# Kernel tuning notes

Measured on AMD Instinct MI355X. Metric: run time of the kernel, lower is better.

## Reference

```python
import jax, jax.numpy as jnp
import numpy as np

B = 8
H1c = W1c = 56
H2c = W2c = 112
C1 = 512
C2 = 256
NH = 8
WS = 7
POOL = 2
EPS = 1e-5


def setup_inputs() -> dict:
    key = jax.random.key(0)
    ks = jax.random.split(key, 8)
    x = jax.random.normal(ks[0], (B, H1c * W1c, C1), dtype=jnp.float32)
    y = jax.random.normal(ks[1], (B, H2c * W2c, C2), dtype=jnp.float32)
    Wq = jax.random.normal(ks[2], (C1, C1), dtype=jnp.float32) * 0.02
    Wkv = jax.random.normal(ks[3], (2 * C1, C2), dtype=jnp.float32) * 0.02
    Wproj = jax.random.normal(ks[4], (C1, C1), dtype=jnp.float32) * 0.02
    bproj = jnp.zeros((C1,), dtype=jnp.float32)
    # 1x1 conv: fan_out = out_channels -> std = sqrt(2/C2)
    Wsr = jax.random.normal(ks[5], (C2, C2), dtype=jnp.float32) * np.sqrt(2.0 / C2).astype(np.float32)
    bsr = jnp.zeros((C2,), dtype=jnp.float32)
    gn = jnp.ones((C2,), dtype=jnp.float32)
    bn = jnp.zeros((C2,), dtype=jnp.float32)
    return {"x": x, "y": y, "Wq": Wq, "Wkv": Wkv, "Wproj": Wproj,
            "bproj": bproj, "Wsr": Wsr, "bsr": bsr, "gn": gn, "bn": bn,
            "H1": H1c, "W1": W1c, "H2": H2c, "W2": W2c}


def _window_partition(t, ws):
    # t: (B, nh, H, W, C) -> (B*nh, num_windows, ws*ws, C)
    Bt, n, H, W, C = t.shape
    ht, wt = H // ws, W // ws
    t = t.reshape(Bt, n, ht, ws, wt, ws, C).transpose(0, 1, 2, 4, 3, 5, 6)
    return t.reshape(Bt * n, ht * wt, ws * ws, C)


def reference(x, y, Wq, Wkv, Wproj, bproj, Wsr, bsr, gn, bn, H1, W1, H2, W2):
    B1, N1, c1 = x.shape
    B2, N2, c2 = y.shape
    nh, ws = NH, WS
    hd = c1 // nh
    scale = hd ** (-0.5)

    # q projection -> (B, nh, H1, W1, hd)
    q = (x @ Wq.T).reshape(B1, H1, W1, nh, hd).transpose(0, 3, 1, 2, 4)

    # KV preprocessing: avgpool -> 1x1 conv -> layernorm -> gelu
    y2 = y.transpose(0, 2, 1).reshape(B2, c2, H2, W2)
    Hp, Wp = H2 // POOL, W2 // POOL
    y2 = y2.reshape(B2, c2, Hp, POOL, Wp, POOL).mean(axis=(3, 5))
    y2 = jnp.einsum('bchw,oc->bohw', y2, Wsr) + bsr[None, :, None, None]
    y2 = y2.reshape(B2, c2, Hp * Wp).transpose(0, 2, 1)  # (B, Np, C2)
    mu = y2.mean(-1, keepdims=True)
    var = y2.var(-1, keepdims=True)
    y2 = (y2 - mu) / jnp.sqrt(var + EPS) * gn + bn
    y2 = jax.nn.gelu(y2, approximate=False)

    kv = (y2 @ Wkv.T).reshape(B2, Hp * Wp, 2, nh, hd)
    k = kv[:, :, 0].transpose(0, 2, 1, 3).reshape(B2, nh, Hp, Wp, hd)
    v = kv[:, :, 1].transpose(0, 2, 1, 3).reshape(B2, nh, Hp, Wp, hd)

    qw = _window_partition(q, ws)   # (B*nh, nw, ws^2, hd)
    kw = _window_partition(k, ws)
    vw = _window_partition(v, ws)

    attn = jax.nn.softmax(jnp.einsum('bnqd,bnkd->bnqk', qw, kw) * scale, axis=-1)
    out = jnp.einsum('bnqk,bnkd->bnqd', attn, vw)  # (B*nh, nw, ws^2, hd)

    # window reverse -> (B, N1, C1)
    ht, wt = H1 // ws, W1 // ws
    out = out.reshape(B1, nh, ht, wt, ws, ws, hd).transpose(0, 1, 2, 4, 3, 5, 6)
    out = out.reshape(B1, nh, H1 * W1, hd).transpose(0, 2, 1, 3).reshape(B1, H1 * W1, c1)
    return out @ Wproj.T + bproj
```

## Files before the change

### kernel.cpp

```cpp
#include <hip/hip_runtime.h>
#include <hip/hip_bf16.h>

typedef __attribute__((ext_vector_type(8))) short short8;
typedef __attribute__((ext_vector_type(4))) float f32x4;
typedef __attribute__((ext_vector_type(4))) unsigned short ushort4v;

#define DI __device__ __forceinline__

DI unsigned short f2bf(float f) {
  union { float f; unsigned int u; } a; a.f = f;
  unsigned int u = a.u;
  return (unsigned short)((u + 0x7FFFu + ((u >> 16) & 1u)) >> 16);
}

#define BARRIER() do { asm volatile("" ::: "memory"); __builtin_amdgcn_s_barrier(); asm volatile("" ::: "memory"); } while (0)
#define GLOAD16(src, dst) __builtin_amdgcn_global_load_lds( \
    (const __attribute__((address_space(1))) void*)(src), \
    (__attribute__((address_space(3))) void*)(dst), 16, 0, 0)


__global__ __launch_bounds__(256)
void cvt_pool(const float* __restrict__ y, unsigned short* __restrict__ pooled,
              const float* __restrict__ Wq, const float* __restrict__ Wkv,
              const float* __restrict__ Wproj, const float* __restrict__ Wsr,
              unsigned short* __restrict__ Wq_b, unsigned short* __restrict__ Wkv_b,
              unsigned short* __restrict__ Wproj_b, unsigned short* __restrict__ Wsr_b) {
  int bid = blockIdx.x;
  if (bid < 6272) {
    int t = bid * 256 + threadIdx.x;
    int cv = (t & 63) * 4;
    int bp = t >> 6;
    int b = bp / 3136, p = bp % 3136;
    int hp = p / 56, wp = p % 56;
    const float* src = y + (((size_t)b * 12544) + hp * 224 + wp * 2) * 256 + cv;
    float4 a0 = *(const float4*)(src);
    float4 a1 = *(const float4*)(src + 256);
    float4 a2 = *(const float4*)(src + 28672);
    float4 a3 = *(const float4*)(src + 28672 + 256);
    float4 av;
    av.x = (a0.x + a1.x + a2.x + a3.x) * 0.25f;
    av.y = (a0.y + a1.y + a2.y + a3.y) * 0.25f;
    av.z = (a0.z + a1.z + a2.z + a3.z) * 0.25f;
    av.w = (a0.w + a1.w + a2.w + a3.w) * 0.25f;
    ushort4v o = { f2bf(av.x), f2bf(av.y), f2bf(av.z), f2bf(av.w) };
    *(ushort4v*)&pooled[(size_t)bp * 256 + cv] = o;
  } else {
    long i = (long)(bid - 6272) * 1024 + threadIdx.x * 4;
    const float* src; unsigned short* dst; long off;
    if (i < 262144L)      { src = Wq;    dst = Wq_b;    off = i; }
    else if (i < 524288L) { src = Wkv;   dst = Wkv_b;   off = i - 262144L; }
    else if (i < 786432L) { src = Wproj; dst = Wproj_b; off = i - 524288L; }
    else                  { src = Wsr;   dst = Wsr_b;   off = i - 786432L; }
    float4 v = *(const float4*)&src[off];
    ushort4v o = { f2bf(v.x), f2bf(v.y), f2bf(v.z), f2bf(v.w) };
    *(ushort4v*)&dst[off] = o;
  }
}

__global__ __launch_bounds__(256)
void sr_gemm(const unsigned short* __restrict__ Ap, const unsigned short* __restrict__ Wsr_b,
             const float* __restrict__ bsr, const float* __restrict__ gn,
             const float* __restrict__ bn, unsigned short* __restrict__ out) {
  __shared__ unsigned short sA[64 * 64];
  __shared__ unsigned short sB[256 * 64];
  __shared__ float red[64 * 8];

  const int tid = threadIdx.x;
  const int wv = tid >> 6;
  const int lane = tid & 63;
  const int lr = lane & 15;
  const int lg = lane >> 4;
  const int lr4 = lg * 4;
  const int m0 = blockIdx.x * 64;
  const int sr8 = lane >> 3;
  const int sl8 = lane & 7;

  f32x4 acc[4][4];
#pragma unroll
  for (int i = 0; i < 4; ++i)
#pragma unroll
    for (int j = 0; j < 4; ++j) acc[i][j] = (f32x4){0.f, 0.f, 0.f, 0.f};

  for (int kt = 0; kt < 256; kt += 64) {
#pragma unroll
    for (int c = 0; c < 2; ++c) {
      int row = wv * 16 + c * 8 + sr8;
      GLOAD16(Ap + (size_t)(m0 + row) * 256 + kt + ((sl8 ^ (row & 7)) * 8),
              &sA[(wv * 16 + c * 8) * 64]);
    }
#pragma unroll
    for (int c = 0; c < 8; ++c) {
      int row = wv * 64 + c * 8 + sr8;
      GLOAD16(Wsr_b + (size_t)row * 256 + kt + ((sl8 ^ (row & 7)) * 8),
              &sB[(wv * 64 + c * 8) * 64]);
    }
    __syncthreads();
#pragma unroll
    for (int ks = 0; ks < 2; ++ks) {
      short8 af[4], bfr[4];
#pragma unroll
      for (int i = 0; i < 4; ++i)
        af[i] = *(const short8*)&sA[(i * 16 + lr) * 64 + (((ks * 4 + lg) ^ (lr & 7)) * 8)];
#pragma unroll
      for (int j = 0; j < 4; ++j)
        bfr[j] = *(const short8*)&sB[(wv * 64 + j * 16 + lr) * 64 + (((ks * 4 + lg) ^ (lr & 7)) * 8)];
#pragma unroll
      for (int i = 0; i < 4; ++i)
#pragma unroll
        for (int j = 0; j < 4; ++j)
          acc[i][j] = __builtin_amdgcn_mfma_f32_16x16x32_bf16(af[i], bfr[j], acc[i][j], 0, 0, 0);
    }
    __syncthreads();
  }

  float bsv[4], gnv[4], bnv[4];
#pragma unroll
  for (int j = 0; j < 4; ++j) {
    int col = wv * 64 + j * 16 + lr;
    bsv[j] = bsr[col]; gnv[j] = gn[col]; bnv[j] = bn[col];
  }
  float s_[4][4], q_[4][4];
#pragma unroll
  for (int i = 0; i < 4; ++i)
#pragma unroll
    for (int r = 0; r < 4; ++r) {
      float s = 0.f, q = 0.f;
#pragma unroll
      for (int j = 0; j < 4; ++j) {
        float v = acc[i][j][r] + bsv[j];
        acc[i][j][r] = v;
        s += v; q += v * v;
      }
      s_[i][r] = s; q_[i][r] = q;
    }
#pragma unroll
  for (int m = 1; m <= 8; m <<= 1)
#pragma unroll
    for (int i = 0; i < 4; ++i)
#pragma unroll
      for (int r = 0; r < 4; ++r) {
        s_[i][r] += __shfl_xor(s_[i][r], m);
        q_[i][r] += __shfl_xor(q_[i][r], m);
      }
  if (lr == 0) {
#pragma unroll
    for (int i = 0; i < 4; ++i)
#pragma unroll
      for (int r = 0; r < 4; ++r) {
        int row = i * 16 + lr4 + r;
        red[row * 8 + wv * 2 + 0] = s_[i][r];
        red[row * 8 + wv * 2 + 1] = q_[i][r];
      }
  }
  __syncthreads();
#pragma unroll
  for (int i = 0; i < 4; ++i) {
#pragma unroll
    for (int r = 0; r < 4; ++r) {
      int row = i * 16 + lr4 + r;
      float sum = red[row * 8 + 0] + red[row * 8 + 2] + red[row * 8 + 4] + red[row * 8 + 6];
      float sq  = red[row * 8 + 1] + red[row * 8 + 3] + red[row * 8 + 5] + red[row * 8 + 7];
      float mean = sum * (1.f / 256.f);
      float var = sq * (1.f / 256.f) - mean * mean;
      float rstd = rsqrtf(var + 1e-5f);
#pragma unroll
      for (int j = 0; j < 4; ++j) {
        float t = (acc[i][j][r] - mean) * rstd * gnv[j] + bnv[j];
        t = 0.5f * t * (1.f + erff(t * 0.70710678118654752f));
        out[(size_t)(m0 + row) * 256 + wv * 64 + j * 16 + lr] = f2bf(t);
      }
    }
  }
}

template<int N, int EPI>
DI void epi_store(int gm, int gc, float v, void* outp, const float* bias, unsigned short* out2) {
  if constexpr (EPI == 3) {
    ((float*)outp)[(size_t)gm * N + gc] = v + bias[gc];
  } else if constexpr (EPI == 0) {
    const int b = gm / 3136, pos = gm % 3136;
    const int h = pos / 56, ww = pos % 56;
    const int head = gc >> 6, d = gc & 63;
    const size_t idx = ((((size_t)(b * 8 + head)) * 64 + (h / 7) * 8 + (ww / 7)) * 49
                        + (h % 7) * 7 + (ww % 7)) * 64 + d;
    ((unsigned short*)outp)[idx] = f2bf(v);
  }
}

template<int K, int N, int EPI>
__global__ __launch_bounds__(512, 2)
void gemm256f(const float* __restrict__ A,
              const unsigned short* __restrict__ Bw,
              void* __restrict__ outp,
              const float* __restrict__ bias,
              unsigned short* __restrict__ out2) {
  __shared__ unsigned short lds[65536];
  const int tid = threadIdx.x;
  const int wv = tid >> 6;
  const int lane = tid & 63;
  const int wm = wv >> 2;
  const int wn = wv & 3;
  const int m0 = blockIdx.y * 256;
  const int n0 = blockIdx.x * 256;
  const int lr = lane & 15;
  const int lg = lane >> 4;
  const int lr4 = lg * 4;
  const int srow8 = lane >> 3;
  const int sl8 = lane & 7;
  constexpr int NT = K / 64;

  f32x4 acc[8][4];
#pragma unroll
  for (int i = 0; i < 8; ++i)
#pragma unroll
    for (int j = 0; j < 4; ++j) acc[i][j] = (f32x4){0.f, 0.f, 0.f, 0.f};

  float4 fa[4][2];
  auto loadA = [&](int t1) {
    int tsrc = (t1 < NT) ? t1 : NT - 1;
#pragma unroll
    for (int rr = 0; rr < 4; ++rr) {
      int trow = rr * 64 + wv * 8 + srow8;
      const float* p = A + (size_t)(m0 + trow) * K + tsrc * 64 + sl8 * 8;
      fa[rr][0] = *(const float4*)p;
      fa[rr][1] = *(const float4*)(p + 4);
    }
    asm volatile("" ::: "memory");
  };
  auto writeA = [&](int t1) {
#pragma unroll
    for (int rr = 0; rr < 4; ++rr) {
      int trow = rr * 64 + wv * 8 + srow8;
      union { short8 s; unsigned short u[8]; } w;
      w.u[0] = f2bf(fa[rr][0].x); w.u[1] = f2bf(fa[rr][0].y);
      w.u[2] = f2bf(fa[rr][0].z); w.u[3] = f2bf(fa[rr][0].w);
      w.u[4] = f2bf(fa[rr][1].x); w.u[5] = f2bf(fa[rr][1].y);
      w.u[6] = f2bf(fa[rr][1].z); w.u[7] = f2bf(fa[rr][1].w);
      *(short8*)&lds[(t1 & 1) * 32768 + trow * 64 + ((sl8 ^ (trow & 7)) * 8)] = w.s;
    }
  };
  auto stageB = [&](int t1, int rr) {
    int tsrc = (t1 < NT) ? t1 : NT - 1;
    int trow = rr * 64 + wv * 8 + srow8;
    int sx = sl8 ^ (trow & 7);
    GLOAD16(Bw + (size_t)(n0 + trow) * K + tsrc * 64 + sx * 8,
            &lds[(t1 & 1) * 32768 + 16384 + (rr * 64 + wv * 8) * 64]);
  };
  auto rdA = [&](int s, int mf, int ks) -> short8 {
    int row = wm * 128 + mf * 16 + lr;
    int slot = ((ks << 2) + lg) ^ (row & 7);
    return *(const short8*)&lds[s * 32768 + row * 64 + slot * 8];
  };
  auto rdB = [&](int s, int nf, int ks) -> short8 {
    int row = wn * 64 + nf * 16 + lr;
    int slot = ((ks << 2) + lg) ^ (row & 7);
    return *(const short8*)&lds[s * 32768 + 16384 + row * 64 + slot * 8];
  };

  stageB(0, 0); stageB(0, 1); stageB(0, 2); stageB(0, 3);
  loadA(0);
  asm volatile("s_waitcnt vmcnt(0)" ::: "memory");
  writeA(0);
  asm volatile("s_waitcnt lgkmcnt(0)" ::: "memory");
  BARRIER();

  for (int t = 0; t < NT; ++t) {
    const int s = t & 1;
    short8 bfr[4][2];
    loadA(t + 1);
#pragma unroll
    for (int j = 0; j < 4; ++j) { bfr[j][0] = rdB(s, j, 0); bfr[j][1] = rdB(s, j, 1); }
    {
      short8 x0 = rdA(s, 0, 0), x1 = rdA(s, 0, 1);
      short8 y0 = rdA(s, 1, 0), y1 = rdA(s, 1, 1);
      BARRIER();
      __builtin_amdgcn_s_setprio(1);
#pragma unroll
      for (int j = 0; j < 4; ++j) {
        acc[0][j] = __builtin_amdgcn_mfma_f32_16x16x32_bf16(x0, bfr[j][0], acc[0][j], 0, 0, 0);
        acc[0][j] = __builtin_amdgcn_mfma_f32_16x16x32_bf16(x1, bfr[j][1], acc[0][j], 0, 0, 0);
        acc[1][j] = __builtin_amdgcn_mfma_f32_16x16x32_bf16(y0, bfr[j][0], acc[1][j], 0, 0, 0);
        acc[1][j] = __builtin_amdgcn_mfma_f32_16x16x32_bf16(y1, bfr[j][1], acc[1][j], 0, 0, 0);
      }
      __builtin_amdgcn_s_setprio(0);
      BARRIER();
    }
    stageB(t + 1, 0); stageB(t + 1, 1);
    {
      short8 x0 = rdA(s, 2, 0), x1 = rdA(s, 2, 1);
      short8 y0 = rdA(s, 3, 0), y1 = rdA(s, 3, 1);
      BARRIER();
      __builtin_amdgcn_s_setprio(1);
#pragma unroll
      for (int j = 0; j < 4; ++j) {
        acc[2][j] = __builtin_amdgcn_mfma_f32_16x16x32_bf16(x0, bfr[j][0], acc[2][j], 0, 0, 0);
        acc[2][j] = __builtin_amdgcn_mfma_f32_16x16x32_bf16(x1, bfr[j][1], acc[2][j], 0, 0, 0);
        acc[3][j] = __builtin_amdgcn_mfma_f32_16x16x32_bf16(y0, bfr[j][0], acc[3][j], 0, 0, 0);
        acc[3][j] = __builtin_amdgcn_mfma_f32_16x16x32_bf16(y1, bfr[j][1], acc[3][j], 0, 0, 0);
      }
      __builtin_amdgcn_s_setprio(0);
      BARRIER();
    }
    stageB(t + 1, 2); stageB(t + 1, 3);
    {
      short8 x0 = rdA(s, 4, 0), x1 = rdA(s, 4, 1);
      short8 y0 = rdA(s, 5, 0), y1 = rdA(s, 5, 1);
      BARRIER();
      __builtin_amdgcn_s_setprio(1);
#pragma unroll
      for (int j = 0; j < 4; ++j) {
        acc[4][j] = __builtin_amdgcn_mfma_f32_16x16x32_bf16(x0, bfr[j][0], acc[4][j], 0, 0, 0);
        acc[4][j] = __builtin_amdgcn_mfma_f32_16x16x32_bf16(x1, bfr[j][1], acc[4][j], 0, 0, 0);
        acc[5][j] = __builtin_amdgcn_mfma_f32_16x16x32_bf16(y0, bfr[j][0], acc[5][j], 0, 0, 0);
        acc[5][j] = __builtin_amdgcn_mfma_f32_16x16x32_bf16(y1, bfr[j][1], acc[5][j], 0, 0, 0);
      }
      __builtin_amdgcn_s_setprio(0);
      BARRIER();
    }
    {
      short8 x0 = rdA(s, 6, 0), x1 = rdA(s, 6, 1);
      short8 y0 = rdA(s, 7, 0), y1 = rdA(s, 7, 1);
      asm volatile("s_waitcnt vmcnt(4)" ::: "memory");
      writeA(t + 1);
      asm volatile("s_waitcnt lgkmcnt(0)" ::: "memory");
      BARRIER();
      __builtin_amdgcn_s_setprio(1);
#pragma unroll
      for (int j = 0; j < 4; ++j) {
        acc[6][j] = __builtin_amdgcn_mfma_f32_16x16x32_bf16(x0, bfr[j][0], acc[6][j], 0, 0, 0);
        acc[6][j] = __builtin_amdgcn_mfma_f32_16x16x32_bf16(x1, bfr[j][1], acc[6][j], 0, 0, 0);
        acc[7][j] = __builtin_amdgcn_mfma_f32_16x16x32_bf16(y0, bfr[j][0], acc[7][j], 0, 0, 0);
        acc[7][j] = __builtin_amdgcn_mfma_f32_16x16x32_bf16(y1, bfr[j][1], acc[7][j], 0, 0, 0);
      }
      __builtin_amdgcn_s_setprio(0);
      asm volatile("s_waitcnt vmcnt(0)" ::: "memory");
      BARRIER();
    }
  }

#pragma unroll
  for (int i = 0; i < 8; ++i)
#pragma unroll
    for (int j = 0; j < 4; ++j)
#pragma unroll
      for (int r = 0; r < 4; ++r)
        epi_store<N, EPI>(m0 + wm * 128 + i * 16 + lr4 + r, n0 + wn * 64 + j * 16 + lr,
                          acc[i][j][r], outp, bias, out2);
}

__global__ __launch_bounds__(512)
void kvattn(const unsigned short* __restrict__ y2,
            const unsigned short* __restrict__ Wkv_b,
            const unsigned short* __restrict__ qwin,
            const unsigned short* __restrict__ Wproj_b,
            const float* __restrict__ bproj,
            float* __restrict__ out) {
  __shared__ unsigned short W_[32768];
  __shared__ unsigned short Br[32768];
  __shared__ unsigned short Cy[16384];

  const int tid = threadIdx.x;
  const int wv = tid >> 6;
  const int lane = tid & 63;
  const int lr = lane & 15;
  const int lg = lane >> 4;
  const int r8 = lane >> 3;
  const int sl8 = lane & 7;
  const int bb = blockIdx.x >> 6;
  const int win = blockIdx.x & 63;
  const int ht = win >> 3, wt = win & 7;

  {
    int m = wv * 8 + r8;
    int mm = (m < 49) ? m : 48;
    int grow = bb * 3136 + (ht * 7 + mm / 7) * 56 + wt * 7 + (mm % 7);
#pragma unroll
    for (int kt = 0; kt < 4; ++kt)
      GLOAD16(y2 + (size_t)grow * 256 + kt * 64 + ((sl8 ^ (m & 7)) * 8),
              &Cy[kt * 4096 + wv * 8 * 64]);
  }

  f32x4 aK[4][4], aV[4][4];
#pragma unroll
  for (int i = 0; i < 4; ++i)
#pragma unroll
    for (int j = 0; j < 4; ++j) { aK[i][j] = (f32x4){0,0,0,0}; aV[i][j] = (f32x4){0,0,0,0}; }

#pragma unroll
  for (int h2 = 0; h2 < 2; ++h2) {
    for (int kt = 0; kt < 4; ++kt) {
#pragma unroll
      for (int c = 0; c < 8; ++c) {
        int nrow = c * 64 + wv * 8 + r8;
        GLOAD16(Wkv_b + (size_t)(h2 * 512 + nrow) * 256 + kt * 64 + ((sl8 ^ (nrow & 7)) * 8),
                &W_[(c * 64 + wv * 8) * 64]);
      }
      __syncthreads();
      short8 bfrg[4][2];
#pragma unroll
      for (int nf = 0; nf < 4; ++nf)
#pragma unroll
        for (int ks = 0; ks < 2; ++ks) {
          int row = wv * 64 + nf * 16 + lr;
          bfrg[nf][ks] = *(const short8*)&W_[row * 64 + (((ks * 4 + lg) ^ (row & 7)) * 8)];
        }
#pragma unroll
      for (int mf = 0; mf < 4; ++mf)
#pragma unroll
        for (int ks = 0; ks < 2; ++ks) {
          int arow = mf * 16 + lr;
          short8 af = *(const short8*)&Cy[kt * 4096 + arow * 64 + (((ks * 4 + lg) ^ (arow & 7)) * 8)];
#pragma unroll
          for (int nf = 0; nf < 4; ++nf) {
            if (h2 == 0)
              aK[mf][nf] = __builtin_amdgcn_mfma_f32_16x16x32_bf16(af, bfrg[nf][ks], aK[mf][nf], 0, 0, 0);
            else
              aV[mf][nf] = __builtin_amdgcn_mfma_f32_16x16x32_bf16(af, bfrg[nf][ks], aV[mf][nf], 0, 0, 0);
          }
        }
      __syncthreads();
    }
  }

#pragma unroll
  for (int mf = 0; mf < 4; ++mf)
#pragma unroll
    for (int nf = 0; nf < 4; ++nf)
#pragma unroll
      for (int r = 0; r < 4; ++r) {
        int key = mf * 16 + lg * 4 + r;
        int d = nf * 16 + lr;
        Br[wv * 4096 + key * 64 + (((d >> 3) ^ (key & 7)) * 8) + (d & 7)] = f2bf(aK[mf][nf][r]);
        W_[wv * 4096 + d * 64 + (((key >> 3) ^ (d & 7)) * 8) + (key & 7)] = f2bf(aV[mf][nf][r]);
      }

  const unsigned short* qb = qwin + (size_t)((bb * 8 + wv) * 64 + win) * 3136;
  f32x4 aS[4][4];
#pragma unroll
  for (int i = 0; i < 4; ++i)
#pragma unroll
    for (int j = 0; j < 4; ++j) aS[i][j] = (f32x4){0,0,0,0};
#pragma unroll
  for (int mf = 0; mf < 4; ++mf)
#pragma unroll
    for (int ks = 0; ks < 2; ++ks) {
      short8 af = *(const short8*)&qb[(mf * 16 + lr) * 64 + ks * 32 + lg * 8];
#pragma unroll
      for (int nf = 0; nf < 4; ++nf) {
        int row = nf * 16 + lr;
        short8 bk = *(const short8*)&Br[wv * 4096 + row * 64 + (((ks * 4 + lg) ^ (row & 7)) * 8)];
        aS[mf][nf] = __builtin_amdgcn_mfma_f32_16x16x32_bf16(af, bk, aS[mf][nf], 0, 0, 0);
      }
    }

#pragma unroll
  for (int nf = 0; nf < 4; ++nf)
    if (nf * 16 + lr >= 49) {
#pragma unroll
      for (int mf = 0; mf < 4; ++mf)
#pragma unroll
        for (int r = 0; r < 4; ++r) aS[mf][nf][r] = -1e30f;
    }
  const float cexp = 0.125f * 1.4426950408889634f;
  float mx[4][4], sm[4][4];
#pragma unroll
  for (int mf = 0; mf < 4; ++mf)
#pragma unroll
    for (int r = 0; r < 4; ++r)
      mx[mf][r] = fmaxf(fmaxf(aS[mf][0][r], aS[mf][1][r]), fmaxf(aS[mf][2][r], aS[mf][3][r]));
#pragma unroll
  for (int m = 1; m <= 8; m <<= 1)
#pragma unroll
    for (int mf = 0; mf < 4; ++mf)
#pragma unroll
      for (int r = 0; r < 4; ++r) mx[mf][r] = fmaxf(mx[mf][r], __shfl_xor(mx[mf][r], m));
#pragma unroll
  for (int mf = 0; mf < 4; ++mf)
#pragma unroll
    for (int nf = 0; nf < 4; ++nf)
#pragma unroll
      for (int r = 0; r < 4; ++r)
        aS[mf][nf][r] = exp2f((aS[mf][nf][r] - mx[mf][r]) * cexp);
#pragma unroll
  for (int mf = 0; mf < 4; ++mf)
#pragma unroll
    for (int r = 0; r < 4; ++r)
      sm[mf][r] = aS[mf][0][r] + aS[mf][1][r] + aS[mf][2][r] + aS[mf][3][r];
#pragma unroll
  for (int m = 1; m <= 8; m <<= 1)
#pragma unroll
    for (int mf = 0; mf < 4; ++mf)
#pragma unroll
      for (int r = 0; r < 4; ++r) sm[mf][r] += __shfl_xor(sm[mf][r], m);
#pragma unroll
  for (int mf = 0; mf < 4; ++mf)
#pragma unroll
    for (int r = 0; r < 4; ++r) sm[mf][r] = 1.f / sm[mf][r];

#pragma unroll
  for (int mf = 0; mf < 4; ++mf)
#pragma unroll
    for (int nf = 0; nf < 4; ++nf)
#pragma unroll
      for (int r = 0; r < 4; ++r) {
        int q = mf * 16 + lg * 4 + r;
        int key = nf * 16 + lr;
        Br[wv * 4096 + q * 64 + (((key >> 3) ^ (q & 7)) * 8) + (key & 7)] =
            f2bf(aS[mf][nf][r] * sm[mf][r]);
      }

  f32x4 aO[4][4];
#pragma unroll
  for (int i = 0; i < 4; ++i)
#pragma unroll
    for (int j = 0; j < 4; ++j) aO[i][j] = (f32x4){0,0,0,0};
#pragma unroll
  for (int mf = 0; mf < 4; ++mf)
#pragma unroll
    for (int ks = 0; ks < 2; ++ks) {
      int qrow = mf * 16 + lr;
      short8 pf = *(const short8*)&Br[wv * 4096 + qrow * 64 + (((ks * 4 + lg) ^ (qrow & 7)) * 8)];
#pragma unroll
      for (int df = 0; df < 4; ++df) {
        int drow = df * 16 + lr;
        short8 vf = *(const short8*)&W_[wv * 4096 + drow * 64 + (((ks * 4 + lg) ^ (drow & 7)) * 8)];
        aO[mf][df] = __builtin_amdgcn_mfma_f32_16x16x32_bf16(pf, vf, aO[mf][df], 0, 0, 0);
      }
    }

  __syncthreads();
#pragma unroll
  for (int mf = 0; mf < 4; ++mf)
#pragma unroll
    for (int nf = 0; nf < 4; ++nf)
#pragma unroll
      for (int r = 0; r < 4; ++r) {
        int q = mf * 16 + lg * 4 + r;
        int slot = nf * 2 + (lr >> 3);
        Br[q * 512 + wv * 64 + ((slot ^ (q & 7)) * 8) + (lr & 7)] = f2bf(aO[mf][nf][r]);
      }
  __syncthreads();

  f32x4 aR[4][4];
#pragma unroll
  for (int i = 0; i < 4; ++i)
#pragma unroll
    for (int j = 0; j < 4; ++j) aR[i][j] = (f32x4){0,0,0,0};
  for (int kt = 0; kt < 8; ++kt) {
#pragma unroll
    for (int c = 0; c < 8; ++c) {
      int nrow = c * 64 + wv * 8 + r8;
      GLOAD16(Wproj_b + (size_t)nrow * 512 + kt * 64 + ((sl8 ^ (nrow & 7)) * 8),
              &W_[(c * 64 + wv * 8) * 64]);
    }
    __syncthreads();
#pragma unroll
    for (int mf = 0; mf < 4; ++mf)
#pragma unroll
      for (int ks = 0; ks < 2; ++ks) {
        int qrow = mf * 16 + lr;
        short8 af = *(const short8*)&Br[qrow * 512 + kt * 64 + (((ks * 4 + lg) ^ (qrow & 7)) * 8)];
#pragma unroll
        for (int nf = 0; nf < 4; ++nf) {
          int nrow = wv * 64 + nf * 16 + lr;
          short8 bf2 = *(const short8*)&W_[nrow * 64 + (((ks * 4 + lg) ^ (nrow & 7)) * 8)];
          aR[mf][nf] = __builtin_amdgcn_mfma_f32_16x16x32_bf16(af, bf2, aR[mf][nf], 0, 0, 0);
        }
      }
    __syncthreads();
  }

#pragma unroll
  for (int mf = 0; mf < 4; ++mf)
#pragma unroll
    for (int nf = 0; nf < 4; ++nf)
#pragma unroll
      for (int r = 0; r < 4; ++r) {
        int q = mf * 16 + lg * 4 + r;
        if (q < 49) {
          int gm = bb * 3136 + (ht * 7 + q / 7) * 56 + wt * 7 + (q % 7);
          int col = wv * 64 + nf * 16 + lr;
          out[(size_t)gm * 512 + col] = aR[mf][nf][r] + bproj[col];
        }
      }
}

extern "C" void kernel_launch(void* const* d_in, const int* in_sizes, int n_in,
                              void* d_out, int out_size, void* d_ws, size_t ws_size,
                              hipStream_t stream) {
  const float* x     = (const float*)d_in[0];
  const float* y     = (const float*)d_in[1];
  const float* Wq    = (const float*)d_in[2];
  const float* Wkv   = (const float*)d_in[3];
  const float* Wproj = (const float*)d_in[4];
  const float* bproj = (const float*)d_in[5];
  const float* Wsr   = (const float*)d_in[6];
  const float* bsr   = (const float*)d_in[7];
  const float* gn    = (const float*)d_in[8];
  const float* bn    = (const float*)d_in[9];
  float* out = (float*)d_out;

  char* ws = (char*)d_ws;
  unsigned short* Wq_b    = (unsigned short*)ws; ws += 524288;
  unsigned short* Wkv_b   = (unsigned short*)ws; ws += 524288;
  unsigned short* Wproj_b = (unsigned short*)ws; ws += 524288;
  unsigned short* Wsr_b   = (unsigned short*)ws; ws += 131072;
  unsigned short* regA    = (unsigned short*)ws; ws += 12845056;
  unsigned short* q_win   = (unsigned short*)ws; ws += 25690112;
  unsigned short* regC    = (unsigned short*)ws; ws += 12845056;

  cvt_pool<<<7104, 256, 0, stream>>>(y, regA, Wq, Wkv, Wproj, Wsr,
                                     Wq_b, Wkv_b, Wproj_b, Wsr_b);

  gemm256f<512, 512, 0><<<dim3(2, 98), 512, 0, stream>>>(x, Wq_b, q_win, nullptr, nullptr);

  sr_gemm<<<392, 256, 0, stream>>>(regA, Wsr_b, bsr, gn, bn, regC);

  kvattn<<<512, 512, 0, stream>>>(regC, Wkv_b, q_win, Wproj_b, bproj, out);
}
```

Baseline: 160.6 us.

## Give each wave private double-buffered weight staging in kvattn to drop block barriers

The fused KV-projection/attention/output-projection kernel now stages Wkv tiles per wave into private, double-buffered LDS slices, loading the next stage while the current one is consumed. This removes the block-wide __syncthreads that every k-step used to need. Q fragments are prefetched into registers before the K/V stores, and the Wproj loop uses register prefetch of the next tile into a per-wave LDS slice instead of block-synchronised global-to-LDS loads. LDS regions are aliased carefully, which relies on the remaining barriers for correctness. The GEMM epilogue template is simplified as cleanup.

```diff
diff --git a/kernel.cpp b/kernel.cpp
--- a/kernel.cpp
+++ b/kernel.cpp
@@ -173,27 +173,20 @@
   }
 }
 
-template<int N, int EPI>
-DI void epi_store(int gm, int gc, float v, void* outp, const float* bias, unsigned short* out2) {
-  if constexpr (EPI == 3) {
-    ((float*)outp)[(size_t)gm * N + gc] = v + bias[gc];
-  } else if constexpr (EPI == 0) {
-    const int b = gm / 3136, pos = gm % 3136;
-    const int h = pos / 56, ww = pos % 56;
-    const int head = gc >> 6, d = gc & 63;
-    const size_t idx = ((((size_t)(b * 8 + head)) * 64 + (h / 7) * 8 + (ww / 7)) * 49
-                        + (h % 7) * 7 + (ww % 7)) * 64 + d;
-    ((unsigned short*)outp)[idx] = f2bf(v);
-  }
+DI void epi_q(int gm, int gc, float v, unsigned short* outp) {
+  const int b = gm / 3136, pos = gm % 3136;
+  const int h = pos / 56, ww = pos % 56;
+  const int head = gc >> 6, d = gc & 63;
+  const size_t idx = ((((size_t)(b * 8 + head)) * 64 + (h / 7) * 8 + (ww / 7)) * 49
+                      + (h % 7) * 7 + (ww % 7)) * 64 + d;
+  outp[idx] = f2bf(v);
 }
 
-template<int K, int N, int EPI>
+template<int K, int N>
 __global__ __launch_bounds__(512, 2)
 void gemm256f(const float* __restrict__ A,
               const unsigned short* __restrict__ Bw,
-              void* __restrict__ outp,
-              const float* __restrict__ bias,
-              unsigned short* __restrict__ out2) {
+              unsigned short* __restrict__ outp) {
   __shared__ unsigned short lds[65536];
   const int tid = threadIdx.x;
   const int wv = tid >> 6;
@@ -344,8 +337,8 @@
     for (int j = 0; j < 4; ++j)
 #pragma unroll
       for (int r = 0; r < 4; ++r)
-        epi_store<N, EPI>(m0 + wm * 128 + i * 16 + lr4 + r, n0 + wn * 64 + j * 16 + lr,
-                          acc[i][j][r], outp, bias, out2);
+        epi_q(m0 + wm * 128 + i * 16 + lr4 + r, n0 + wn * 64 + j * 16 + lr,
+              acc[i][j][r], outp);
 }
 
 __global__ __launch_bounds__(512)
@@ -355,10 +348,7 @@
             const unsigned short* __restrict__ Wproj_b,
             const float* __restrict__ bproj,
             float* __restrict__ out) {
-  __shared__ unsigned short W_[32768];
-  __shared__ unsigned short Br[32768];
-  __shared__ unsigned short Cy[16384];
-
+  __shared__ unsigned short lds[81920];
   const int tid = threadIdx.x;
   const int wv = tid >> 6;
   const int lane = tid & 63;
@@ -370,6 +360,11 @@
   const int win = blockIdx.x & 63;
   const int ht = win >> 3, wt = win & 7;
 
+  unsigned short* Cy = lds;
+  unsigned short* SL = lds + 16384 + wv * 8192;
+  unsigned short* OA = lds + 16384;
+  unsigned short* WP = lds + 49152 + wv * 4096;
+
   {
     int m = wv * 8 + r8;
     int mm = (m < 49) ? m : 48;
@@ -380,47 +375,64 @@
               &Cy[kt * 4096 + wv * 8 * 64]);
   }
 
+  auto stageW = [&](int s) {
+    int h2 = s >> 2, kt = s & 3;
+#pragma unroll
+    for (int c = 0; c < 8; ++c) {
+      int lrow = c * 8 + r8;
+      GLOAD16(Wkv_b + (size_t)(h2 * 512 + wv * 64 + lrow) * 256 + kt * 64 + ((sl8 ^ (lrow & 7)) * 8),
+              &SL[(s & 1) * 4096 + c * 8 * 64]);
+    }
+  };
+
   f32x4 aK[4][4], aV[4][4];
 #pragma unroll
   for (int i = 0; i < 4; ++i)
 #pragma unroll
     for (int j = 0; j < 4; ++j) { aK[i][j] = (f32x4){0,0,0,0}; aV[i][j] = (f32x4){0,0,0,0}; }
 
-#pragma unroll
-  for (int h2 = 0; h2 < 2; ++h2) {
-    for (int kt = 0; kt < 4; ++kt) {
-#pragma unroll
-      for (int c = 0; c < 8; ++c) {
-        int nrow = c * 64 + wv * 8 + r8;
-        GLOAD16(Wkv_b + (size_t)(h2 * 512 + nrow) * 256 + kt * 64 + ((sl8 ^ (nrow & 7)) * 8),
-                &W_[(c * 64 + wv * 8) * 64]);
-      }
-      __syncthreads();
-      short8 bfrg[4][2];
-#pragma unroll
-      for (int nf = 0; nf < 4; ++nf)
-#pragma unroll
-        for (int ks = 0; ks < 2; ++ks) {
-          int row = wv * 64 + nf * 16 + lr;
-          bfrg[nf][ks] = *(const short8*)&W_[row * 64 + (((ks * 4 + lg) ^ (row & 7)) * 8)];
+  stageW(0);
+  asm volatile("s_waitcnt vmcnt(8)" ::: "memory");
+  BARRIER();
+
+#pragma unroll
+  for (int s = 0; s < 8; ++s) {
+    if (s < 7) {
+      stageW(s + 1);
+      asm volatile("s_waitcnt vmcnt(8)" ::: "memory");
+    } else {
+      asm volatile("s_waitcnt vmcnt(0)" ::: "memory");
+    }
+    const int kt = s & 3;
+    const unsigned short* Wb = &SL[(s & 1) * 4096];
+    short8 bfrg[4][2];
+#pragma unroll
+    for (int nf = 0; nf < 4; ++nf)
+#pragma unroll
+      for (int ks = 0; ks < 2; ++ks)
+        bfrg[nf][ks] = *(const short8*)&Wb[(nf * 16 + lr) * 64 + (((ks * 4 + lg) ^ (lr & 7)) * 8)];
+#pragma unroll
+    for (int mf = 0; mf < 4; ++mf)
+#pragma unroll
+      for (int ks = 0; ks < 2; ++ks) {
+        short8 af = *(const short8*)&Cy[kt * 4096 + (mf * 16 + lr) * 64 + (((ks * 4 + lg) ^ (lr & 7)) * 8)];
+#pragma unroll
+        for (int nf = 0; nf < 4; ++nf) {
+          if (s < 4)
+            aK[mf][nf] = __builtin_amdgcn_mfma_f32_16x16x32_bf16(af, bfrg[nf][ks], aK[mf][nf], 0, 0, 0);
+          else
+            aV[mf][nf] = __builtin_amdgcn_mfma_f32_16x16x32_bf16(af, bfrg[nf][ks], aV[mf][nf], 0, 0, 0);
         }
-#pragma unroll
-      for (int mf = 0; mf < 4; ++mf)
-#pragma unroll
-        for (int ks = 0; ks < 2; ++ks) {
-          int arow = mf * 16 + lr;
-          short8 af = *(const short8*)&Cy[kt * 4096 + arow * 64 + (((ks * 4 + lg) ^ (arow & 7)) * 8)];
-#pragma unroll
-          for (int nf = 0; nf < 4; ++nf) {
-            if (h2 == 0)
-              aK[mf][nf] = __builtin_amdgcn_mfma_f32_16x16x32_bf16(af, bfrg[nf][ks], aK[mf][nf], 0, 0, 0);
-            else
-              aV[mf][nf] = __builtin_amdgcn_mfma_f32_16x16x32_bf16(af, bfrg[nf][ks], aV[mf][nf], 0, 0, 0);
-          }
-        }
-      __syncthreads();
-    }
-  }
+      }
+  }
+
+  const unsigned short* qb = qwin + (size_t)((bb * 8 + wv) * 64 + win) * 3136;
+  short8 qf[4][2];
+#pragma unroll
+  for (int mf = 0; mf < 4; ++mf)
+#pragma unroll
+    for (int ks = 0; ks < 2; ++ks)
+      qf[mf][ks] = *(const short8*)&qb[(mf * 16 + lr) * 64 + ks * 32 + lg * 8];
 
 #pragma unroll
   for (int mf = 0; mf < 4; ++mf)
@@ -430,11 +442,10 @@
       for (int r = 0; r < 4; ++r) {
         int key = mf * 16 + lg * 4 + r;
         int d = nf * 16 + lr;
-        Br[wv * 4096 + key * 64 + (((d >> 3) ^ (key & 7)) * 8) + (d & 7)] = f2bf(aK[mf][nf][r]);
-        W_[wv * 4096 + d * 64 + (((key >> 3) ^ (d & 7)) * 8) + (key & 7)] = f2bf(aV[mf][nf][r]);
-      }
-
-  const unsigned short* qb = qwin + (size_t)((bb * 8 + wv) * 64 + win) * 3136;
+        SL[key * 64 + (((d >> 3) ^ (key & 7)) * 8) + (d & 7)] = f2bf(aK[mf][nf][r]);
+        SL[4096 + d * 64 + (((key >> 3) ^ (d & 7)) * 8) + (key & 7)] = f2bf(aV[mf][nf][r]);
+      }
+
   f32x4 aS[4][4];
 #pragma unroll
   for (int i = 0; i < 4; ++i)
@@ -443,15 +454,12 @@
 #pragma unroll
   for (int mf = 0; mf < 4; ++mf)
 #pragma unroll
-    for (int ks = 0; ks < 2; ++ks) {
-      short8 af = *(const short8*)&qb[(mf * 16 + lr) * 64 + ks * 32 + lg * 8];
+    for (int ks = 0; ks < 2; ++ks)
 #pragma unroll
       for (int nf = 0; nf < 4; ++nf) {
-        int row = nf * 16 + lr;
-        short8 bk = *(const short8*)&Br[wv * 4096 + row * 64 + (((ks * 4 + lg) ^ (row & 7)) * 8)];
-        aS[mf][nf] = __builtin_amdgcn_mfma_f32_16x16x32_bf16(af, bk, aS[mf][nf], 0, 0, 0);
-      }
-    }
+        short8 bk = *(const short8*)&SL[(nf * 16 + lr) * 64 + (((ks * 4 + lg) ^ (lr & 7)) * 8)];
+        aS[mf][nf] = __builtin_amdgcn_mfma_f32_16x16x32_bf16(qf[mf][ks], bk, aS[mf][nf], 0, 0, 0);
+      }
 
 #pragma unroll
   for (int nf = 0; nf < 4; ++nf)
@@ -505,8 +513,7 @@
       for (int r = 0; r < 4; ++r) {
         int q = mf * 16 + lg * 4 + r;
         int key = nf * 16 + lr;
-        Br[wv * 4096 + q * 64 + (((key >> 3) ^ (q & 7)) * 8) + (key & 7)] =
-            f2bf(aS[mf][nf][r] * sm[mf][r]);
+        SL[q * 64 + (((key >> 3) ^ (q & 7)) * 8) + (key & 7)] = f2bf(aS[mf][nf][r] * sm[mf][r]);
       }
 
   f32x4 aO[4][4];
@@ -518,17 +525,15 @@
   for (int mf = 0; mf < 4; ++mf)
 #pragma unroll
     for (int ks = 0; ks < 2; ++ks) {
-      int qrow = mf * 16 + lr;
-      short8 pf = *(const short8*)&Br[wv * 4096 + qrow * 64 + (((ks * 4 + lg) ^ (qrow & 7)) * 8)];
+      short8 pf = *(const short8*)&SL[(mf * 16 + lr) * 64 + (((ks * 4 + lg) ^ (lr & 7)) * 8)];
 #pragma unroll
       for (int df = 0; df < 4; ++df) {
-        int drow = df * 16 + lr;
-        short8 vf = *(const short8*)&W_[wv * 4096 + drow * 64 + (((ks * 4 + lg) ^ (drow & 7)) * 8)];
+        short8 vf = *(const short8*)&SL[4096 + (df * 16 + lr) * 64 + (((ks * 4 + lg) ^ (lr & 7)) * 8)];
         aO[mf][df] = __builtin_amdgcn_mfma_f32_16x16x32_bf16(pf, vf, aO[mf][df], 0, 0, 0);
       }
     }
 
-  __syncthreads();
+  BARRIER();
 #pragma unroll
   for (int mf = 0; mf < 4; ++mf)
 #pragma unroll
@@ -537,37 +542,52 @@
       for (int r = 0; r < 4; ++r) {
         int q = mf * 16 + lg * 4 + r;
         int slot = nf * 2 + (lr >> 3);
-        Br[q * 512 + wv * 64 + ((slot ^ (q & 7)) * 8) + (lr & 7)] = f2bf(aO[mf][nf][r]);
-      }
-  __syncthreads();
+        OA[q * 512 + wv * 64 + ((slot ^ (q & 7)) * 8) + (lr & 7)] = f2bf(aO[mf][nf][r]);
+      }
+  {
+    short8 nx[8];
+#pragma unroll
+    for (int c = 0; c < 8; ++c) {
+      int lrow = c * 8 + r8;
+      nx[c] = *(const short8*)&Wproj_b[(size_t)(wv * 64 + lrow) * 512 + ((sl8 ^ (lrow & 7)) * 8)];
+    }
+#pragma unroll
+    for (int c = 0; c < 8; ++c)
+      *(short8*)&WP[(c * 8 + r8) * 64 + sl8 * 8] = nx[c];
+  }
+  BARRIER();
 
   f32x4 aR[4][4];
 #pragma unroll
   for (int i = 0; i < 4; ++i)
 #pragma unroll
     for (int j = 0; j < 4; ++j) aR[i][j] = (f32x4){0,0,0,0};
+#pragma unroll
   for (int kt = 0; kt < 8; ++kt) {
-#pragma unroll
-    for (int c = 0; c < 8; ++c) {
-      int nrow = c * 64 + wv * 8 + r8;
-      GLOAD16(Wproj_b + (size_t)nrow * 512 + kt * 64 + ((sl8 ^ (nrow & 7)) * 8),
-              &W_[(c * 64 + wv * 8) * 64]);
-    }
-    __syncthreads();
+    short8 nx[8];
+    if (kt < 7) {
+#pragma unroll
+      for (int c = 0; c < 8; ++c) {
+        int lrow = c * 8 + r8;
+        nx[c] = *(const short8*)&Wproj_b[(size_t)(wv * 64 + lrow) * 512 + (kt + 1) * 64 + ((sl8 ^ (lrow & 7)) * 8)];
+      }
+    }
 #pragma unroll
     for (int mf = 0; mf < 4; ++mf)
 #pragma unroll
       for (int ks = 0; ks < 2; ++ks) {
-        int qrow = mf * 16 + lr;
-        short8 af = *(const short8*)&Br[qrow * 512 + kt * 64 + (((ks * 4 + lg) ^ (qrow & 7)) * 8)];
+        short8 af = *(const short8*)&OA[(mf * 16 + lr) * 512 + kt * 64 + (((ks * 4 + lg) ^ (lr & 7)) * 8)];
 #pragma unroll
         for (int nf = 0; nf < 4; ++nf) {
-          int nrow = wv * 64 + nf * 16 + lr;
-          short8 bf2 = *(const short8*)&W_[nrow * 64 + (((ks * 4 + lg) ^ (nrow & 7)) * 8)];
+          short8 bf2 = *(const short8*)&WP[(nf * 16 + lr) * 64 + (((ks * 4 + lg) ^ (lr & 7)) * 8)];
           aR[mf][nf] = __builtin_amdgcn_mfma_f32_16x16x32_bf16(af, bf2, aR[mf][nf], 0, 0, 0);
         }
       }
-    __syncthreads();
+    if (kt < 7) {
+#pragma unroll
+      for (int c = 0; c < 8; ++c)
+        *(short8*)&WP[(c * 8 + r8) * 64 + sl8 * 8] = nx[c];
+    }
   }
 
 #pragma unroll
@@ -612,7 +632,7 @@
   cvt_pool<<<7104, 256, 0, stream>>>(y, regA, Wq, Wkv, Wproj, Wsr,
                                      Wq_b, Wkv_b, Wproj_b, Wsr_b);
 
-  gemm256f<512, 512, 0><<<dim3(2, 98), 512, 0, stream>>>(x, Wq_b, q_win, nullptr, nullptr);
+  gemm256f<512, 512><<<dim3(2, 98), 512, 0, stream>>>(x, Wq_b, q_win);
 
   sr_gemm<<<392, 256, 0, stream>>>(regA, Wsr_b, bsr, gn, bn, regC);
 
```

After: 141.4 us. -12.0%, faster.
